# Performance work log

Measured on AMD Instinct MI355X. Metric: run time of the kernel, lower is better.

The kernel has to match this reference:

```python
import jax, jax.numpy as jnp
import numpy as np

D_MODEL = 768
D_STATE = 16
D_CONV = 4
EXPAND = 2
D_INNER = EXPAND * D_MODEL          # 1536
DT_RANK = (D_MODEL + 15) // 16      # 48
B, L = 2, 1024


def _mamba_params(key):
    ks = jax.random.split(key, 8)
    s = 0.02
    return dict(
        in_w=jax.random.normal(ks[0], (2 * D_INNER, D_MODEL), jnp.float32) * s,
        conv_w=jax.random.normal(ks[1], (D_INNER, D_CONV), jnp.float32) * s,
        conv_b=jnp.zeros((D_INNER,), jnp.float32),
        xproj_w=jax.random.normal(ks[2], (DT_RANK + 2 * D_STATE, D_INNER), jnp.float32) * s,
        dt_w=jax.random.normal(ks[3], (D_INNER, DT_RANK), jnp.float32) * s,
        dt_b=jax.random.normal(ks[4], (D_INNER,), jnp.float32) * s,
        A_log=jnp.broadcast_to(jnp.log(jnp.arange(1, D_STATE + 1, dtype=jnp.float32)), (D_INNER, D_STATE)).copy(),
        D=jnp.ones((D_INNER,), jnp.float32),
        out_w=jax.random.normal(ks[5], (D_MODEL, D_INNER), jnp.float32) * s,
    )


def setup_inputs() -> dict:
    key = jax.random.key(0)
    kx, kf, kb = jax.random.split(key, 3)
    inp = {
        'x': jax.random.normal(kx, (B, L, D_MODEL), jnp.float32),
        'ln_g': jnp.ones((D_MODEL,), jnp.float32),
        'ln_b': jnp.zeros((D_MODEL,), jnp.float32),
    }
    for pref, k in (('f_', kf), ('b_', kb)):
        for name, v in _mamba_params(k).items():
            inp[pref + name] = v
    return inp


def _layernorm(x, g, b, eps=1e-5):
    m = x.mean(-1, keepdims=True)
    v = ((x - m) ** 2).mean(-1, keepdims=True)
    return (x - m) * jax.lax.rsqrt(v + eps) * g + b


def _mamba(x, in_w, conv_w, conv_b, xproj_w, dt_w, dt_b, A_log, Dp, out_w):
    # x: (B, L, d_model)
    xz = x @ in_w.T                             # (B, L, 2*d_inner)
    xc, z = jnp.split(xz, 2, axis=-1)
    # depthwise causal conv1d over time
    xt = xc.transpose(0, 2, 1)                  # (B, d_inner, L)
    k = conv_w[:, None, :]                      # (d_inner, 1, d_conv)
    conv = jax.lax.conv_general_dilated(
        xt, k, (1,), [(D_CONV - 1, 0)],
        feature_group_count=D_INNER,
        dimension_numbers=('NCH', 'OIH', 'NCH'))
    xc = jax.nn.silu((conv + conv_b[None, :, None]).transpose(0, 2, 1))  # (B, L, d_inner)
    # input-dependent SSM parameters
    dbc = xc @ xproj_w.T                        # (B, L, dt_rank + 2*d_state)
    dt, Bm, Cm = jnp.split(dbc, [DT_RANK, DT_RANK + D_STATE], axis=-1)
    delta = jax.nn.softplus(dt @ dt_w.T + dt_b)  # (B, L, d_inner)
    A = -jnp.exp(A_log)                          # (d_inner, d_state)
    dA = jnp.exp(delta[..., None] * A)           # (B, L, d_inner, d_state)
    dBu = delta[..., None] * Bm[:, :, None, :] * xc[..., None]

    def step(h, inp):
        dA_t, dBu_t, C_t = inp                   # (B,d,n), (B,d,n), (B,n)
        h = dA_t * h + dBu_t
        return h, jnp.einsum('bdn,bn->bd', h, C_t)

    h0 = jnp.zeros((xc.shape[0], D_INNER, D_STATE), xc.dtype)
    _, ys = jax.lax.scan(step, h0,
                         (dA.transpose(1, 0, 2, 3), dBu.transpose(1, 0, 2, 3), Cm.transpose(1, 0, 2)))
    y = ys.transpose(1, 0, 2) + xc * Dp          # skip via D
    y = y * jax.nn.silu(z)                       # gate
    return y @ out_w.T


def reference(x, ln_g, ln_b,
              f_in_w, f_conv_w, f_conv_b, f_xproj_w, f_dt_w, f_dt_b, f_A_log, f_D, f_out_w,
              b_in_w, b_conv_w, b_conv_b, b_xproj_w, b_dt_w, b_dt_b, b_A_log, b_D, b_out_w):
    x0 = _layernorm(x, ln_g, ln_b)
    fwd = _mamba(x0, f_in_w, f_conv_w, f_conv_b, f_xproj_w, f_dt_w, f_dt_b, f_A_log, f_D, f_out_w)
    bwd = _mamba(jnp.flip(x0, 1), b_in_w, b_conv_w, b_conv_b, b_xproj_w, b_dt_w, b_dt_b, b_A_log, b_D, b_out_w)
    out = fwd + jnp.flip(bwd, 1)
    return x + out  # dropout is identity in eval mode
```

## Files before the change

### kernel.cpp

```cpp
#include <hip/hip_runtime.h>


typedef unsigned short u16;
typedef unsigned int u32;
typedef __bf16 bf16x8 __attribute__((ext_vector_type(8)));
typedef float f32x4 __attribute__((ext_vector_type(4)));
typedef u32 u32x4 __attribute__((ext_vector_type(4)));

#define L_SEQ 1024
#define DM 768
#define DI 1536
#define DS 16
#define DTR 48
#define M_TOK 2048
#define TCH 64
#define NCH (L_SEQ / TCH)
#define GP 4

__device__ __forceinline__ float bf2f(u16 u) {
  union { u32 i; float f; } v; v.i = ((u32)u) << 16; return v.f;
}
__device__ __forceinline__ u16 f2bf(float f) {
  union { float f; u32 i; } v; v.f = f;
  u32 r = v.i + 0x7fffu + ((v.i >> 16) & 1u);
  return (u16)(r >> 16);
}

__launch_bounds__(256)
__global__ void k_cvt(const float* __restrict__ in, u16* __restrict__ out, int n) {
  const int i = blockIdx.x * 256 + threadIdx.x;
  if (i < n) out[i] = f2bf(in[i]);
}

__launch_bounds__(256)
__global__ void k_ln(const float* __restrict__ x, const float* __restrict__ g,
                     const float* __restrict__ b, u16* __restrict__ x0) {
  const int tok = blockIdx.x;
  const int tid = threadIdx.x;
  const float e0 = x[tok * DM + tid];
  const float e1 = x[tok * DM + tid + 256];
  const float e2 = x[tok * DM + tid + 512];
  float s = e0 + e1 + e2;
  float s2 = e0 * e0 + e1 * e1 + e2 * e2;
#pragma unroll
  for (int off = 1; off < 64; off <<= 1) {
    s += __shfl_xor(s, off, 64);
    s2 += __shfl_xor(s2, off, 64);
  }
  __shared__ float rs[4], rq[4];
  const int wave = tid >> 6, lane = tid & 63;
  if (lane == 0) { rs[wave] = s; rq[wave] = s2; }
  __syncthreads();
  s = rs[0] + rs[1] + rs[2] + rs[3];
  s2 = rq[0] + rq[1] + rq[2] + rq[3];
  const float mean = s * (1.0f / DM);
  const float var = s2 * (1.0f / DM) - mean * mean;
  const float inv = rsqrtf(var + 1e-5f);
  x0[tok * DM + tid]       = f2bf((e0 - mean) * inv * g[tid]       + b[tid]);
  x0[tok * DM + tid + 256] = f2bf((e1 - mean) * inv * g[tid + 256] + b[tid + 256]);
  x0[tok * DM + tid + 512] = f2bf((e2 - mean) * inv * g[tid + 512] + b[tid + 512]);
}

__launch_bounds__(256)
__global__ void k_pad_xproj(const float* __restrict__ w0, const float* __restrict__ w1,
                            u16* __restrict__ o0, u16* __restrict__ o1) {
  const int dir = blockIdx.z;
  const float* w = dir ? w1 : w0;
  u16* o = dir ? o1 : o0;
  const int col = blockIdx.x * 256 + threadIdx.x;
  const int row = blockIdx.y;
  o[row * DI + col] = (row < 80) ? f2bf(w[row * DI + col]) : (u16)0;
}
__launch_bounds__(256)
__global__ void k_pad_dtw(const float* __restrict__ w0, const float* __restrict__ w1,
                          u16* __restrict__ o0, u16* __restrict__ o1) {
  const int dir = blockIdx.y;
  const float* w = dir ? w1 : w0;
  u16* o = dir ? o1 : o0;
  const int idx = blockIdx.x * 256 + threadIdx.x;
  const int row = idx >> 6, col = idx & 63;
  o[idx] = (col < DTR) ? f2bf(w[row * DTR + col]) : (u16)0;
}

template <int BN, int WN, int MODE>
__launch_bounds__(256)
__global__ void k_gemm(const u16* __restrict__ A0, const u16* __restrict__ A1,
                       const u16* __restrict__ W0, const u16* __restrict__ W1,
                       float* __restrict__ C0, float* __restrict__ C1,
                       const float* __restrict__ b0, const float* __restrict__ b1,
                       u16* __restrict__ aux0, u16* __restrict__ aux1,
                       int N, int K, int flip1) {
  constexpr int NWC = BN / WN;
  constexpr int FJ = WN / 16;
  constexpr int CB = (BN * 32) / (256 * 8);

  const int dir = blockIdx.z;
  const u16* A = dir ? A1 : A0;
  const u16* W = dir ? W1 : W0;
  float* C = dir ? C1 : C0;
  const float* bias = dir ? b1 : b0;
  u16* aux = dir ? aux1 : aux0;
  const int doflip = flip1 & dir;

  __shared__ __align__(16) u16 sA[128 * 32];
  __shared__ __align__(16) u16 sB[BN * 32];

  const int tid = threadIdx.x;
  const int lane = tid & 63, wave = tid >> 6;
  const int m0 = blockIdx.y * 128, n0 = blockIdx.x * BN;

  const f32x4 vzero = {0.f, 0.f, 0.f, 0.f};
  f32x4 acc[4][FJ];
#pragma unroll
  for (int i = 0; i < 4; ++i)
#pragma unroll
    for (int j = 0; j < FJ; ++j) acc[i][j] = vzero;

  const int lrow = lane & 15, kseg = lane >> 4;
  const int wm = (wave / NWC) * 64, wn = (wave % NWC) * WN;

  u32x4 va[2][2], vb[2][CB];

#define GLOAD(s, kt)                                                          \
  {                                                                           \
    _Pragma("unroll") for (int c = 0; c < 2; ++c) {                           \
      const int q = c * 256 + tid;                                            \
      int rA = m0 + (q >> 2);                                                 \
      if (doflip) rA ^= (L_SEQ - 1);                                          \
      va[s][c] = *(const u32x4*)(A + (size_t)rA * K + (kt) + (q & 3) * 8);    \
    }                                                                         \
    _Pragma("unroll") for (int c = 0; c < CB; ++c) {                          \
      const int q = c * 256 + tid;                                            \
      vb[s][c] = *(const u32x4*)(W + (size_t)(n0 + (q >> 2)) * K + (kt) +     \
                                 (q & 3) * 8);                                \
    }                                                                         \
  }
#define SSTORE(s)                                                             \
  {                                                                           \
    _Pragma("unroll") for (int c = 0; c < 2; ++c)                             \
        *(u32x4*)&sA[(c * 256 + tid) * 8] = va[s][c];                         \
    _Pragma("unroll") for (int c = 0; c < CB; ++c)                            \
        *(u32x4*)&sB[(c * 256 + tid) * 8] = vb[s][c];                         \
  }
#define COMPUTE()                                                             \
  {                                                                           \
    bf16x8 af[4], bfv[FJ];                                                    \
    _Pragma("unroll") for (int i = 0; i < 4; ++i)                             \
        af[i] = *(const bf16x8*)&sA[(wm + i * 16 + lrow) * 32 + kseg * 8];    \
    _Pragma("unroll") for (int j = 0; j < FJ; ++j)                            \
        bfv[j] = *(const bf16x8*)&sB[(wn + j * 16 + lrow) * 32 + kseg * 8];   \
    _Pragma("unroll") for (int i = 0; i < 4; ++i)                             \
        _Pragma("unroll") for (int j = 0; j < FJ; ++j)                        \
            acc[i][j] = __builtin_amdgcn_mfma_f32_16x16x32_bf16(              \
                af[i], bfv[j], acc[i][j], 0, 0, 0);                           \
  }

  GLOAD(0, 0)
  for (int kt = 0; kt < K; kt += 64) {
    __syncthreads();
    SSTORE(0)
    __syncthreads();
    GLOAD(1, kt + 32)
    COMPUTE()
    __syncthreads();
    SSTORE(1)
    __syncthreads();
    if (kt + 64 < K) GLOAD(0, kt + 64)
    COMPUTE()
  }
#undef GLOAD
#undef SSTORE
#undef COMPUTE

  const int erow = (lane >> 4) * 4, ecol = lane & 15;
#pragma unroll
  for (int i = 0; i < 4; ++i) {
#pragma unroll
    for (int j = 0; j < FJ; ++j) {
#pragma unroll
      for (int r = 0; r < 4; ++r) {
        const int m = m0 + wm + i * 16 + erow + r;
        const int n = n0 + wn + j * 16 + ecol;
        float v = acc[i][j][r];
        if (MODE == 2) {
          const float xv = v + bias[n];
          v = fmaxf(xv, 0.f) + log1pf(__expf(-fabsf(xv)));
        }
        C[(size_t)m * N + n] = v;
        if (MODE == 1) {
          if (n < 64) aux[m * 64 + n] = f2bf(n < DTR ? v : 0.f);
        }
      }
    }
  }
}

__launch_bounds__(256)
__global__ void k_conv(const float* __restrict__ xz0, const float* __restrict__ xz1,
                       u16* __restrict__ xc0, u16* __restrict__ xc1,
                       const float* __restrict__ w0, const float* __restrict__ w1,
                       const float* __restrict__ cb0, const float* __restrict__ cb1) {
  const int dir = blockIdx.z;
  const float* xz = dir ? xz1 : xz0;
  u16* xc = dir ? xc1 : xc0;
  const float* w = dir ? w1 : w0;
  const float* cb = dir ? cb1 : cb0;
  const int d = blockIdx.x * 256 + threadIdx.x;
  const int tok = blockIdx.y;
  const int l = tok & (L_SEQ - 1);
  float s = cb[d];
#pragma unroll
  for (int j = 0; j < 4; ++j) {
    const int ls = l - 3 + j;
    if (ls >= 0) s += w[d * 4 + j] * xz[(size_t)(tok - 3 + j) * (2 * DI) + d];
  }
  const float r = s / (1.f + __expf(-s));
  xc[(size_t)tok * DI + d] = f2bf(r);
}

template <int PASS>
__launch_bounds__(64, 4)
__global__ void k_scan_pass(const float* __restrict__ dl0, const float* __restrict__ dl1,
                            const u16* __restrict__ xc0, const u16* __restrict__ xc1,
                            const float* __restrict__ dbc0, const float* __restrict__ dbc1,
                            const float* __restrict__ xz0, const float* __restrict__ xz1,
                            const float* __restrict__ al0, const float* __restrict__ al1,
                            const float* __restrict__ dp0, const float* __restrict__ dp1,
                            float* __restrict__ Sb, float* __restrict__ Pb,
                            const float* __restrict__ Hin,
                            u16* __restrict__ y0, u16* __restrict__ y1) {
  const int bdir = blockIdx.z;
  const int dir = bdir & 1, b = bdir >> 1;
  const float* delta = dir ? dl1 : dl0;
  const u16* xc = dir ? xc1 : xc0;
  const float* dbc = dir ? dbc1 : dbc0;
  const float* xz = dir ? xz1 : xz0;
  const float* alog = dir ? al1 : al0;
  const float* dpp = dir ? dp1 : dp0;
  u16* y = dir ? y1 : y0;

  const int tid = threadIdx.x;
  const int d = blockIdx.x * 64 + tid;
  const int ch = blockIdx.y;
  const size_t tb = (size_t)b * L_SEQ;
  const int t0 = ch * TCH;

  __shared__ float sBC[TCH][32];
#pragma unroll
  for (int p = 0; p < 8; ++p) {
    const int idx = p * 64 + tid;
    const int rb = idx >> 3, cb = (idx & 7) * 4;
    *(f32x4*)&sBC[rb][cb] = *(const f32x4*)&dbc[(tb + t0 + rb) * 128 + 48 + cb];
  }

  float Af[16];
#pragma unroll
  for (int q = 0; q < 4; ++q) {
    const f32x4 a = *(const f32x4*)&alog[d * DS + q * 4];
#pragma unroll
    for (int j = 0; j < 4; ++j) Af[q * 4 + j] = -__expf(a[j]);
  }

  float h[16], Pp[16];
  if (PASS == 1) {
#pragma unroll
    for (int n = 0; n < 16; ++n) { h[n] = 0.f; Pp[n] = 1.f; }
  } else {
#pragma unroll
    for (int n = 0; n < 16; ++n)
      h[n] = Hin[(((size_t)bdir * NCH + ch) * 16 + n) * DI + d];
  }
  const float Dv = (PASS == 2) ? dpp[d] : 0.f;

  __syncthreads();

  float db[2][GP], zb[2][GP];
  u16 xb[2][GP];
#define TLOAD(g, bu)                                                      \
  {                                                                       \
    _Pragma("unroll") for (int i = 0; i < GP; ++i) {                      \
      const size_t row = tb + t0 + (g) * GP + i;                          \
      db[bu][i] = delta[row * DI + d];                                    \
      xb[bu][i] = xc[row * DI + d];                                       \
      if (PASS == 2) zb[bu][i] = xz[row * (2 * DI) + DI + d];             \
    }                                                                     \
  }
  TLOAD(0, 0)
#pragma unroll 1
  for (int g = 0; g < TCH / GP; ++g) {
    const int bu = g & 1;
    if (g + 1 < TCH / GP) TLOAD(g + 1, bu ^ 1)
#pragma unroll
    for (int i = 0; i < GP; ++i) {
      const int t = g * GP + i;
      const float dlt = db[bu][i];
      const float xcv = bf2f(xb[bu][i]);
      const float dbx = dlt * xcv;
      float yv = 0.f;
#pragma unroll
      for (int q = 0; q < 4; ++q) {
        const f32x4 B4 = *(const f32x4*)&sBC[t][q * 4];
        f32x4 C4;
        if (PASS == 2) C4 = *(const f32x4*)&sBC[t][16 + q * 4];
#pragma unroll
        for (int j = 0; j < 4; ++j) {
          const int n = q * 4 + j;
          const float dA = __expf(dlt * Af[n]);
          if (PASS == 1) Pp[n] *= dA;
          h[n] = fmaf(dA, h[n], B4[j] * dbx);
          if (PASS == 2) yv = fmaf(h[n], C4[j], yv);
        }
      }
      if (PASS == 2) {
        const float zv = zb[bu][i];
        const float sz = zv / (1.f + __expf(-zv));
        y[(tb + t0 + t) * DI + d] = f2bf((yv + xcv * Dv) * sz);
      }
    }
  }
#undef TLOAD

  if (PASS == 1) {
#pragma unroll
    for (int n = 0; n < 16; ++n) {
      const size_t o = (((size_t)bdir * NCH + ch) * 16 + n) * DI + d;
      Sb[o] = h[n];
      Pb[o] = Pp[n];
    }
  }
}

__launch_bounds__(256)
__global__ void k_comb(const float* __restrict__ Sb, const float* __restrict__ Pb,
                       float* __restrict__ Hin) {
  const int gid = blockIdx.x * 256 + threadIdx.x;
  const int d = gid % DI;
  const int bn = gid / DI;
  const int bdir = bn >> 4, n = bn & 15;
  float H = 0.f;
#pragma unroll
  for (int c = 0; c < NCH; ++c) {
    const size_t o = (((size_t)bdir * NCH + c) * 16 + n) * DI + d;
    Hin[o] = H;
    H = fmaf(Pb[o], H, Sb[o]);
  }
}

__launch_bounds__(256)
__global__ void k_final(const float* __restrict__ x, const float* __restrict__ g0,
                        const float* __restrict__ g1, float* __restrict__ out) {
  const int c = blockIdx.x * 256 + threadIdx.x;
  const int tok = blockIdx.y;
  const int ftok = tok ^ (L_SEQ - 1);
  const size_t i = (size_t)tok * DM + c;
  out[i] = x[i] + g0[i] + g1[(size_t)ftok * DM + c];
}

extern "C" void kernel_launch(void* const* d_in, const int* in_sizes, int n_in,
                              void* d_out, int out_size, void* d_ws, size_t ws_size,
                              hipStream_t stream) {
  (void)n_in; (void)out_size; (void)in_sizes;
  const float* x      = (const float*)d_in[0];
  const float* ln_g   = (const float*)d_in[1];
  const float* ln_b   = (const float*)d_in[2];
  const float* in_w_f[2]  = {(const float*)d_in[3],  (const float*)d_in[12]};
  const float* conv_w[2]  = {(const float*)d_in[4],  (const float*)d_in[13]};
  const float* conv_b[2]  = {(const float*)d_in[5],  (const float*)d_in[14]};
  const float* xproj_w[2] = {(const float*)d_in[6],  (const float*)d_in[15]};
  const float* dt_w[2]    = {(const float*)d_in[7],  (const float*)d_in[16]};
  const float* dt_b[2]    = {(const float*)d_in[8],  (const float*)d_in[17]};
  const float* A_log[2]   = {(const float*)d_in[9],  (const float*)d_in[18]};
  const float* Dp[2]      = {(const float*)d_in[10], (const float*)d_in[19]};
  const float* out_w_f[2] = {(const float*)d_in[11], (const float*)d_in[20]};

  char* ws = (char*)d_ws;
  size_t off = 0;
  auto alloc = [&](size_t bytes) {
    void* p = ws + off;
    off = (off + bytes + 255) & ~(size_t)255;
    return p;
  };

  u16* inw[2];  for (int i = 0; i < 2; ++i) inw[i]  = (u16*)alloc((size_t)2 * DI * DM * 2);
  u16* outw[2]; for (int i = 0; i < 2; ++i) outw[i] = (u16*)alloc((size_t)DM * DI * 2);
  u16* x0 = (u16*)alloc((size_t)M_TOK * DM * 2);
  float* xz[2];   for (int i = 0; i < 2; ++i) xz[i]   = (float*)alloc((size_t)M_TOK * 2 * DI * 4);
  u16* xc[2];     for (int i = 0; i < 2; ++i) xc[i]   = (u16*)alloc((size_t)M_TOK * DI * 2);
  float* dbc[2];  for (int i = 0; i < 2; ++i) dbc[i]  = (float*)alloc((size_t)M_TOK * 128 * 4);
  u16* dtin[2];   for (int i = 0; i < 2; ++i) dtin[i] = (u16*)alloc((size_t)M_TOK * 64 * 2);
  float* dlt[2];  for (int i = 0; i < 2; ++i) dlt[i]  = (float*)alloc((size_t)M_TOK * DI * 4);
  u16* yb[2];     for (int i = 0; i < 2; ++i) yb[i]   = (u16*)alloc((size_t)M_TOK * DI * 2);
  float* gout[2]; for (int i = 0; i < 2; ++i) gout[i] = (float*)alloc((size_t)M_TOK * DM * 4);
  u16* xpw[2];    for (int i = 0; i < 2; ++i) xpw[i]  = (u16*)alloc((size_t)128 * DI * 2);
  u16* dtwp[2];   for (int i = 0; i < 2; ++i) dtwp[i] = (u16*)alloc((size_t)DI * 64 * 2);

  float* Sb  = gout[0];
  float* Pb  = gout[1];
  float* Hin = (float*)inw[0];

  if (off > ws_size) return;

  for (int i = 0; i < 2; ++i) {
    k_cvt<<<dim3((2 * DI * DM + 255) / 256), dim3(256), 0, stream>>>(in_w_f[i], inw[i], 2 * DI * DM);
    k_cvt<<<dim3((DM * DI + 255) / 256), dim3(256), 0, stream>>>(out_w_f[i], outw[i], DM * DI);
  }

  k_ln<<<dim3(M_TOK), dim3(256), 0, stream>>>(x, ln_g, ln_b, x0);
  k_pad_xproj<<<dim3(6, 128, 2), dim3(256), 0, stream>>>(xproj_w[0], xproj_w[1], xpw[0], xpw[1]);
  k_pad_dtw<<<dim3(384, 2), dim3(256), 0, stream>>>(dt_w[0], dt_w[1], dtwp[0], dtwp[1]);
  k_gemm<128, 64, 0><<<dim3(24, 16, 2), dim3(256), 0, stream>>>(
      x0, x0, inw[0], inw[1], xz[0], xz[1], nullptr, nullptr, nullptr, nullptr,
      2 * DI, DM, 1);
  k_conv<<<dim3(6, M_TOK, 2), dim3(256), 0, stream>>>(
      xz[0], xz[1], xc[0], xc[1], conv_w[0], conv_w[1], conv_b[0], conv_b[1]);
  k_gemm<128, 64, 1><<<dim3(1, 16, 2), dim3(256), 0, stream>>>(
      xc[0], xc[1], xpw[0], xpw[1], dbc[0], dbc[1], nullptr, nullptr, dtin[0], dtin[1],
      128, DI, 0);
  k_gemm<128, 64, 2><<<dim3(12, 16, 2), dim3(256), 0, stream>>>(
      dtin[0], dtin[1], dtwp[0], dtwp[1], dlt[0], dlt[1], dt_b[0], dt_b[1], nullptr, nullptr,
      DI, 64, 0);
  k_scan_pass<1><<<dim3(24, NCH, 4), dim3(64), 0, stream>>>(
      dlt[0], dlt[1], xc[0], xc[1], dbc[0], dbc[1], xz[0], xz[1],
      A_log[0], A_log[1], Dp[0], Dp[1], Sb, Pb, nullptr, nullptr, nullptr);
  k_comb<<<dim3(384), dim3(256), 0, stream>>>(Sb, Pb, Hin);
  k_scan_pass<2><<<dim3(24, NCH, 4), dim3(64), 0, stream>>>(
      dlt[0], dlt[1], xc[0], xc[1], dbc[0], dbc[1], xz[0], xz[1],
      A_log[0], A_log[1], Dp[0], Dp[1], Sb, Pb, Hin, yb[0], yb[1]);
  k_gemm<64, 32, 0><<<dim3(12, 16, 2), dim3(256), 0, stream>>>(
      yb[0], yb[1], outw[0], outw[1], gout[0], gout[1], nullptr, nullptr, nullptr, nullptr,
      DM, DI, 0);
  k_final<<<dim3(3, M_TOK), dim3(256), 0, stream>>>(x, gout[0], gout[1], (float*)d_out);
}
```

Measured before the change: 412.2 us.

## Store xz and delta intermediates in bf16 and halve scan chunk length

The in-projection GEMM output (xz) and the softplus delta output are now written as bf16 rather than fp32, and the conv and scan kernels read them as bf16. This targets the memory traffic of the large intermediates. The scan chunk length drops from 64 to 32 with a larger per-group prefetch, which doubles the number of chunks and so adds parallelism. To make room, the chunk-state buffers move to dedicated workspace, and a full workspace memset is added, which costs extra bandwidth every call and loses some precision.

```diff
diff --git a/kernel.cpp b/kernel.cpp
--- a/kernel.cpp
+++ b/kernel.cpp
@@ -13,9 +13,9 @@
 #define DS 16
 #define DTR 48
 #define M_TOK 2048
-#define TCH 64
+#define TCH 32
 #define NCH (L_SEQ / TCH)
-#define GP 4
+#define GP 8
 
 __device__ __forceinline__ float bf2f(u16 u) {
   union { u32 i; float f; } v; v.i = ((u32)u) << 16; return v.f;
@@ -185,10 +185,14 @@
         if (MODE == 2) {
           const float xv = v + bias[n];
           v = fmaxf(xv, 0.f) + log1pf(__expf(-fabsf(xv)));
-        }
-        C[(size_t)m * N + n] = v;
-        if (MODE == 1) {
-          if (n < 64) aux[m * 64 + n] = f2bf(n < DTR ? v : 0.f);
+          aux[(size_t)m * N + n] = f2bf(v);
+        } else if (MODE == 3) {
+          aux[(size_t)m * N + n] = f2bf(v);
+        } else {
+          C[(size_t)m * N + n] = v;
+          if (MODE == 1) {
+            if (n < 64) aux[m * 64 + n] = f2bf(n < DTR ? v : 0.f);
+          }
         }
       }
     }
@@ -196,12 +200,12 @@
 }
 
 __launch_bounds__(256)
-__global__ void k_conv(const float* __restrict__ xz0, const float* __restrict__ xz1,
+__global__ void k_conv(const u16* __restrict__ xz0, const u16* __restrict__ xz1,
                        u16* __restrict__ xc0, u16* __restrict__ xc1,
                        const float* __restrict__ w0, const float* __restrict__ w1,
                        const float* __restrict__ cb0, const float* __restrict__ cb1) {
   const int dir = blockIdx.z;
-  const float* xz = dir ? xz1 : xz0;
+  const u16* xz = dir ? xz1 : xz0;
   u16* xc = dir ? xc1 : xc0;
   const float* w = dir ? w1 : w0;
   const float* cb = dir ? cb1 : cb0;
@@ -212,7 +216,7 @@
 #pragma unroll
   for (int j = 0; j < 4; ++j) {
     const int ls = l - 3 + j;
-    if (ls >= 0) s += w[d * 4 + j] * xz[(size_t)(tok - 3 + j) * (2 * DI) + d];
+    if (ls >= 0) s += w[d * 4 + j] * bf2f(xz[(size_t)(tok - 3 + j) * (2 * DI) + d]);
   }
   const float r = s / (1.f + __expf(-s));
   xc[(size_t)tok * DI + d] = f2bf(r);
@@ -220,10 +224,10 @@
 
 template <int PASS>
 __launch_bounds__(64, 4)
-__global__ void k_scan_pass(const float* __restrict__ dl0, const float* __restrict__ dl1,
+__global__ void k_scan_pass(const u16* __restrict__ dl0, const u16* __restrict__ dl1,
                             const u16* __restrict__ xc0, const u16* __restrict__ xc1,
                             const float* __restrict__ dbc0, const float* __restrict__ dbc1,
-                            const float* __restrict__ xz0, const float* __restrict__ xz1,
+                            const u16* __restrict__ xz0, const u16* __restrict__ xz1,
                             const float* __restrict__ al0, const float* __restrict__ al1,
                             const float* __restrict__ dp0, const float* __restrict__ dp1,
                             float* __restrict__ Sb, float* __restrict__ Pb,
@@ -231,10 +235,10 @@
                             u16* __restrict__ y0, u16* __restrict__ y1) {
   const int bdir = blockIdx.z;
   const int dir = bdir & 1, b = bdir >> 1;
-  const float* delta = dir ? dl1 : dl0;
+  const u16* delta = dir ? dl1 : dl0;
   const u16* xc = dir ? xc1 : xc0;
   const float* dbc = dir ? dbc1 : dbc0;
-  const float* xz = dir ? xz1 : xz0;
+  const u16* xz = dir ? xz1 : xz0;
   const float* alog = dir ? al1 : al0;
   const float* dpp = dir ? dp1 : dp0;
   u16* y = dir ? y1 : y0;
@@ -247,7 +251,7 @@
 
   __shared__ float sBC[TCH][32];
 #pragma unroll
-  for (int p = 0; p < 8; ++p) {
+  for (int p = 0; p < TCH * 32 / (64 * 4); ++p) {
     const int idx = p * 64 + tid;
     const int rb = idx >> 3, cb = (idx & 7) * 4;
     *(f32x4*)&sBC[rb][cb] = *(const f32x4*)&dbc[(tb + t0 + rb) * 128 + 48 + cb];
@@ -274,13 +278,12 @@
 
   __syncthreads();
 
-  float db[2][GP], zb[2][GP];
-  u16 xb[2][GP];
+  u16 du[2][GP], xb[2][GP], zb[2][GP];
 #define TLOAD(g, bu)                                                      \
   {                                                                       \
     _Pragma("unroll") for (int i = 0; i < GP; ++i) {                      \
       const size_t row = tb + t0 + (g) * GP + i;                          \
-      db[bu][i] = delta[row * DI + d];                                    \
+      du[bu][i] = delta[row * DI + d];                                    \
       xb[bu][i] = xc[row * DI + d];                                       \
       if (PASS == 2) zb[bu][i] = xz[row * (2 * DI) + DI + d];             \
     }                                                                     \
@@ -293,7 +296,7 @@
 #pragma unroll
     for (int i = 0; i < GP; ++i) {
       const int t = g * GP + i;
-      const float dlt = db[bu][i];
+      const float dlt = bf2f(du[bu][i]);
       const float xcv = bf2f(xb[bu][i]);
       const float dbx = dlt * xcv;
       float yv = 0.f;
@@ -312,7 +315,7 @@
         }
       }
       if (PASS == 2) {
-        const float zv = zb[bu][i];
+        const float zv = bf2f(zb[bu][i]);
         const float sz = zv / (1.f + __expf(-zv));
         y[(tb + t0 + t) * DI + d] = f2bf((yv + xcv * Dv) * sz);
       }
@@ -384,21 +387,22 @@
   u16* inw[2];  for (int i = 0; i < 2; ++i) inw[i]  = (u16*)alloc((size_t)2 * DI * DM * 2);
   u16* outw[2]; for (int i = 0; i < 2; ++i) outw[i] = (u16*)alloc((size_t)DM * DI * 2);
   u16* x0 = (u16*)alloc((size_t)M_TOK * DM * 2);
-  float* xz[2];   for (int i = 0; i < 2; ++i) xz[i]   = (float*)alloc((size_t)M_TOK * 2 * DI * 4);
+  u16* xzb[2];    for (int i = 0; i < 2; ++i) xzb[i]  = (u16*)alloc((size_t)M_TOK * 2 * DI * 2);
   u16* xc[2];     for (int i = 0; i < 2; ++i) xc[i]   = (u16*)alloc((size_t)M_TOK * DI * 2);
   float* dbc[2];  for (int i = 0; i < 2; ++i) dbc[i]  = (float*)alloc((size_t)M_TOK * 128 * 4);
   u16* dtin[2];   for (int i = 0; i < 2; ++i) dtin[i] = (u16*)alloc((size_t)M_TOK * 64 * 2);
-  float* dlt[2];  for (int i = 0; i < 2; ++i) dlt[i]  = (float*)alloc((size_t)M_TOK * DI * 4);
+  u16* dltb[2];   for (int i = 0; i < 2; ++i) dltb[i] = (u16*)alloc((size_t)M_TOK * DI * 2);
   u16* yb[2];     for (int i = 0; i < 2; ++i) yb[i]   = (u16*)alloc((size_t)M_TOK * DI * 2);
   float* gout[2]; for (int i = 0; i < 2; ++i) gout[i] = (float*)alloc((size_t)M_TOK * DM * 4);
   u16* xpw[2];    for (int i = 0; i < 2; ++i) xpw[i]  = (u16*)alloc((size_t)128 * DI * 2);
   u16* dtwp[2];   for (int i = 0; i < 2; ++i) dtwp[i] = (u16*)alloc((size_t)DI * 64 * 2);
-
-  float* Sb  = gout[0];
-  float* Pb  = gout[1];
-  float* Hin = (float*)inw[0];
+  float* Sb  = (float*)alloc((size_t)4 * NCH * 16 * DI * 4);
+  float* Pb  = (float*)alloc((size_t)4 * NCH * 16 * DI * 4);
+  float* Hin = (float*)alloc((size_t)4 * NCH * 16 * DI * 4);
 
   if (off > ws_size) return;
+
+  hipMemsetAsync(d_ws, 0, off, stream);
 
   for (int i = 0; i < 2; ++i) {
     k_cvt<<<dim3((2 * DI * DM + 255) / 256), dim3(256), 0, stream>>>(in_w_f[i], inw[i], 2 * DI * DM);
@@ -408,23 +412,23 @@
   k_ln<<<dim3(M_TOK), dim3(256), 0, stream>>>(x, ln_g, ln_b, x0);
   k_pad_xproj<<<dim3(6, 128, 2), dim3(256), 0, stream>>>(xproj_w[0], xproj_w[1], xpw[0], xpw[1]);
   k_pad_dtw<<<dim3(384, 2), dim3(256), 0, stream>>>(dt_w[0], dt_w[1], dtwp[0], dtwp[1]);
-  k_gemm<128, 64, 0><<<dim3(24, 16, 2), dim3(256), 0, stream>>>(
-      x0, x0, inw[0], inw[1], xz[0], xz[1], nullptr, nullptr, nullptr, nullptr,
+  k_gemm<128, 64, 3><<<dim3(24, 16, 2), dim3(256), 0, stream>>>(
+      x0, x0, inw[0], inw[1], nullptr, nullptr, nullptr, nullptr, xzb[0], xzb[1],
       2 * DI, DM, 1);
   k_conv<<<dim3(6, M_TOK, 2), dim3(256), 0, stream>>>(
-      xz[0], xz[1], xc[0], xc[1], conv_w[0], conv_w[1], conv_b[0], conv_b[1]);
+      xzb[0], xzb[1], xc[0], xc[1], conv_w[0], conv_w[1], conv_b[0], conv_b[1]);
   k_gemm<128, 64, 1><<<dim3(1, 16, 2), dim3(256), 0, stream>>>(
       xc[0], xc[1], xpw[0], xpw[1], dbc[0], dbc[1], nullptr, nullptr, dtin[0], dtin[1],
       128, DI, 0);
   k_gemm<128, 64, 2><<<dim3(12, 16, 2), dim3(256), 0, stream>>>(
-      dtin[0], dtin[1], dtwp[0], dtwp[1], dlt[0], dlt[1], dt_b[0], dt_b[1], nullptr, nullptr,
+      dtin[0], dtin[1], dtwp[0], dtwp[1], nullptr, nullptr, dt_b[0], dt_b[1], dltb[0], dltb[1],
       DI, 64, 0);
   k_scan_pass<1><<<dim3(24, NCH, 4), dim3(64), 0, stream>>>(
-      dlt[0], dlt[1], xc[0], xc[1], dbc[0], dbc[1], xz[0], xz[1],
+      dltb[0], dltb[1], xc[0], xc[1], dbc[0], dbc[1], xzb[0], xzb[1],
       A_log[0], A_log[1], Dp[0], Dp[1], Sb, Pb, nullptr, nullptr, nullptr);
   k_comb<<<dim3(384), dim3(256), 0, stream>>>(Sb, Pb, Hin);
   k_scan_pass<2><<<dim3(24, NCH, 4), dim3(64), 0, stream>>>(
-      dlt[0], dlt[1], xc[0], xc[1], dbc[0], dbc[1], xz[0], xz[1],
+      dltb[0], dltb[1], xc[0], xc[1], dbc[0], dbc[1], xzb[0], xzb[1],
       A_log[0], A_log[1], Dp[0], Dp[1], Sb, Pb, Hin, yb[0], yb[1]);
   k_gemm<64, 32, 0><<<dim3(12, 16, 2), dim3(256), 0, stream>>>(
       yb[0], yb[1], outw[0], outw[1], gout[0], gout[1], nullptr, nullptr, nullptr, nullptr,
```

Result: slower. 508.6 us (+23.4%).
